# Kernel tuning notes

Hardware: AMD Instinct MI355X
Metric: run time of the kernel (lower is better)

Reference implementation:

```python
import jax, jax.numpy as jnp
import numpy as np
import math

IN_DIM, OUT_DIM, NUM_BASIS = 256, 128, 6
MAX_IN_SEQ, MAX_OUT_SEQ = 512, 256
REDUCTION = 2
LN_EPS = 1e-5


def setup_inputs() -> dict:
    key = jax.random.key(0)
    ks = jax.random.split(key, 8)
    u = lambda k, shape, a: jax.random.uniform(k, shape, jnp.float32, -a, a)
    x = jax.random.normal(ks[0], (16, MAX_IN_SEQ, IN_DIM), jnp.float32)
    M = u(ks[1], (OUT_DIM, IN_DIM), 0.5)
    P = u(ks[2], (OUT_DIM, OUT_DIM, NUM_BASIS), 0.1)
    Linker = u(ks[3], (MAX_IN_SEQ, MAX_OUT_SEQ), 0.1)
    ln_gamma = jnp.ones((OUT_DIM,), jnp.float32)
    ln_beta = jnp.zeros((OUT_DIM,), jnp.float32)
    res_W = u(ks[4], (OUT_DIM, IN_DIM), 0.1)
    res_linker = u(ks[5], (MAX_IN_SEQ, MAX_OUT_SEQ), 0.1)
    # periods[i,j,g] = i*(out_dim*num_basis) + j*num_basis + g + 2 (non-trainable buffer)
    periods = (jnp.arange(OUT_DIM * OUT_DIM * NUM_BASIS, dtype=jnp.float32)
               .reshape(OUT_DIM, OUT_DIM, NUM_BASIS) + 2.0)
    return {"x": x, "M": M, "P": P, "Linker": Linker, "ln_gamma": ln_gamma,
            "ln_beta": ln_beta, "res_W": res_W, "res_linker": res_linker,
            "periods": periods, "actual_seq_len": 512}


def _layer_norm(z, gamma, beta):
    mu = jnp.mean(z, axis=-1, keepdims=True)
    var = jnp.var(z, axis=-1, keepdims=True)
    return (z - mu) * jax.lax.rsqrt(var + LN_EPS) * gamma + beta


def reference(x, M, P, Linker, ln_gamma, ln_beta, res_W, res_linker, periods, actual_seq_len):
    b, seq_len, _ = x.shape
    # Z = LN(x @ M^T)
    Z = _layer_norm(jnp.matmul(x, M.T), ln_gamma, ln_beta)  # (b, s, out)
    # position-dependent trig basis: phi[s,i,j,g] = cos(2*pi*s / periods[i,j,g])
    k = jnp.arange(seq_len, dtype=jnp.float32)[:, None, None, None]
    phi = jnp.cos(2.0 * math.pi * k / periods[None])          # (s, out, out, nb)
    # fold basis into per-position mixing matrix, then contract (matches sum over dims 3,4)
    W = jnp.einsum('ijg,sijg->sij', P, phi)                   # (s, out, out)
    T = jnp.einsum('bsj,sij->bsi', Z, W)                      # (b, s, out)
    # adaptive linker: reduce sequence length
    L = actual_seq_len
    Lo = max(1, L // REDUCTION)
    U = jnp.einsum('bsi,so->boi', T[:, :L], Linker[:L, :Lo])  # (b, out_seq, out)
    # 'separate' residual
    rfeat = jnp.matmul(x[:, :L], res_W.T)                     # (b, s, out)
    residual = jnp.einsum('bsi,so->boi', rfeat, res_linker[:L, :Lo])
    return U + residual
```

## Files before the change

### kernel.cpp

```cpp
#include <hip/hip_runtime.h>
#include <hip/hip_bf16.h>

#define LN_EPS 1e-5f

typedef __attribute__((ext_vector_type(8))) short short8;
typedef __attribute__((ext_vector_type(4))) float floatx4;

__device__ __forceinline__ float bf2f(unsigned int u16) {
    union { unsigned int i; float f; } v; v.i = (u16 & 0xffffu) << 16; return v.f;
}
__device__ __forceinline__ unsigned short f2bf(float f) {
    __hip_bfloat16 h = __float2bfloat16(f);
    union { __hip_bfloat16 h; unsigned short u; } v; v.h = h; return v.u;
}
__device__ __forceinline__ unsigned int pack2(float a, float b) {
    return (unsigned int)f2bf(a) | ((unsigned int)f2bf(b) << 16);
}
__device__ __forceinline__ short8 pack8(float4 a, float4 b) {
    union { short8 s; uint4 u; } v;
    v.u.x = pack2(a.x, a.y); v.u.y = pack2(a.z, a.w);
    v.u.z = pack2(b.x, b.y); v.u.w = pack2(b.z, b.w);
    return v.s;
}

__global__ __launch_bounds__(256) void kB_w_lcat(const float* __restrict__ P,
                                                 const float* __restrict__ periods,
                                                 const float* __restrict__ Linker,
                                                 const float* __restrict__ resL,
                                                 unsigned short* __restrict__ W,
                                                 unsigned short* __restrict__ LcatT) {
    __shared__ unsigned short lds[32 * 260];
    int blk = blockIdx.x, t = threadIdx.x;
    if (blk < 512) {
        int et = blk & 31, sc = blk >> 5;
        int e0 = et * 512 + t * 2;
        const float* pp = P + (size_t)e0 * 6;
        float4 pa = *(const float4*)(pp);
        float4 pb = *(const float4*)(pp + 4);
        float4 pc = *(const float4*)(pp + 8);
        float pf[12] = { pa.x, pa.y, pa.z, pa.w, pb.x, pb.y, pb.z, pb.w, pc.x, pc.y, pc.z, pc.w };
        const float* qp = periods + (size_t)e0 * 6;
        float4 qa = *(const float4*)(qp);
        float4 qb = *(const float4*)(qp + 4);
        float4 qc = *(const float4*)(qp + 8);
        float iv[12] = { __builtin_amdgcn_rcpf(qa.x), __builtin_amdgcn_rcpf(qa.y),
                         __builtin_amdgcn_rcpf(qa.z), __builtin_amdgcn_rcpf(qa.w),
                         __builtin_amdgcn_rcpf(qb.x), __builtin_amdgcn_rcpf(qb.y),
                         __builtin_amdgcn_rcpf(qb.z), __builtin_amdgcn_rcpf(qb.w),
                         __builtin_amdgcn_rcpf(qc.x), __builtin_amdgcn_rcpf(qc.y),
                         __builtin_amdgcn_rcpf(qc.z), __builtin_amdgcn_rcpf(qc.w) };
        float s0 = (float)(sc * 32);
        float tc[12], cm1[12], cc[12];
        #pragma unroll
        for (int g = 0; g < 12; ++g) {
            tc[g]  = 2.0f * __builtin_amdgcn_cosf(iv[g]);
            cm1[g] = __builtin_amdgcn_cosf(__builtin_amdgcn_fractf(s0 * iv[g]));
            cc[g]  = __builtin_amdgcn_cosf(__builtin_amdgcn_fractf((s0 + 1.0f) * iv[g]));
        }
        #pragma unroll 4
        for (int ss = 0; ss < 32; ++ss) {
            float a0 = 0.f, a1 = 0.f;
            #pragma unroll
            for (int g = 0; g < 6; ++g)  a0 += pf[g] * cm1[g];
            #pragma unroll
            for (int g = 6; g < 12; ++g) a1 += pf[g] * cm1[g];
            int s = sc * 32 + ss;
            *(unsigned int*)(W + (size_t)s * 16384 + e0) = pack2(a0, a1);
            #pragma unroll
            for (int g = 0; g < 12; ++g) {
                float cn = fmaf(tc[g], cc[g], -cm1[g]);
                cm1[g] = cc[g]; cc[g] = cn;
            }
        }
    } else {
        int kb = blk - 512;
        int k0 = kb * 32;
        const float* src = (kb < 16) ? (Linker + (size_t)k0 * 256)
                                     : (resL + (size_t)(k0 - 512) * 256);
        #pragma unroll
        for (int q = 0; q < 8; ++q) {
            int lin = t + 256 * q;
            int row = lin >> 6, col4 = (lin & 63) * 4;
            float4 v = *(const float4*)(src + row * 256 + col4);
            *(unsigned int*)(lds + row * 260 + col4)     = pack2(v.x, v.y);
            *(unsigned int*)(lds + row * 260 + col4 + 2) = pack2(v.z, v.w);
        }
        __syncthreads();
        int o = t;
        unsigned int outw[16];
        #pragma unroll
        for (int kp = 0; kp < 16; ++kp) {
            unsigned int lo = lds[(2 * kp) * 260 + o];
            unsigned int hi = lds[(2 * kp + 1) * 260 + o];
            outw[kp] = lo | (hi << 16);
        }
        unsigned short* dst = LcatT + (size_t)o * 1024 + k0;
        #pragma unroll
        for (int qq = 0; qq < 4; ++qq) {
            uint4 u; u.x = outw[qq*4]; u.y = outw[qq*4+1]; u.z = outw[qq*4+2]; u.w = outw[qq*4+3];
            *(uint4*)(dst + qq * 8) = u;
        }
    }
}

__global__ __launch_bounds__(256) void k1_zr(const float* __restrict__ x,
                                             const float* __restrict__ M,
                                             const float* __restrict__ resW,
                                             const float* __restrict__ gamma,
                                             const float* __restrict__ beta,
                                             unsigned short* __restrict__ Z,
                                             unsigned short* __restrict__ TR) {
    __shared__ float buf[32 * 258];
    __shared__ float red1[32 * 8], red2[32 * 8];
    __shared__ float mus[32], rsg[32];
    int t = threadIdx.x, w = t >> 6, l = t & 63;
    int lane15 = l & 15, quad = l >> 4;
    int r0 = blockIdx.x * 32;
    const float* wbase = (w < 2) ? M : resW;
    int wco = (w < 2) ? (w * 64) : (w * 64 - 128);
    floatx4 acc[2][4] = {};
    for (int kk = 0; kk < 256; kk += 32) {
        int k0 = kk + quad * 8;
        const float* xr0 = x + (size_t)(r0 + lane15) * 256 + k0;
        const float* xr1 = x + (size_t)(r0 + 16 + lane15) * 256 + k0;
        short8 a0 = pack8(*(const float4*)xr0, *(const float4*)(xr0 + 4));
        short8 a1 = pack8(*(const float4*)xr1, *(const float4*)(xr1 + 4));
        #pragma unroll
        for (int nt = 0; nt < 4; ++nt) {
            const float* br = wbase + (size_t)(wco + nt * 16 + lane15) * 256 + k0;
            short8 b = pack8(*(const float4*)br, *(const float4*)(br + 4));
            acc[0][nt] = __builtin_amdgcn_mfma_f32_16x16x32_bf16(a0, b, acc[0][nt], 0, 0, 0);
            acc[1][nt] = __builtin_amdgcn_mfma_f32_16x16x32_bf16(a1, b, acc[1][nt], 0, 0, 0);
        }
    }
    #pragma unroll
    for (int mt = 0; mt < 2; ++mt)
        #pragma unroll
        for (int nt = 0; nt < 4; ++nt)
            #pragma unroll
            for (int r = 0; r < 4; ++r) {
                int ro = mt * 16 + quad * 4 + r;
                int co = w * 64 + nt * 16 + lane15;
                buf[ro * 258 + co] = acc[mt][nt][r];
            }
    __syncthreads();
    {
        int r = t >> 3, seg = t & 7;
        float s1 = 0.f, s2 = 0.f;
        #pragma unroll
        for (int e = 0; e < 16; ++e) { float v = buf[r * 258 + seg * 16 + e]; s1 += v; s2 += v * v; }
        red1[r * 8 + seg] = s1; red2[r * 8 + seg] = s2;
    }
    __syncthreads();
    if (t < 32) {
        float s1 = 0.f, s2 = 0.f;
        #pragma unroll
        for (int e = 0; e < 8; ++e) { s1 += red1[t * 8 + e]; s2 += red2[t * 8 + e]; }
        float mu = s1 * (1.0f / 128.0f);
        float var = s2 * (1.0f / 128.0f) - mu * mu;
        mus[t] = mu; rsg[t] = rsqrtf(var + LN_EPS);
    }
    __syncthreads();
    {
        int r = t >> 3, c0 = (t & 7) * 16;
        int grow = r0 + r;
        float mu = mus[r], rs = rsg[r];
        float zv[16], rv[16];
        #pragma unroll
        for (int e = 0; e < 16; ++e) {
            int j = c0 + e;
            zv[e] = (buf[r * 258 + j] - mu) * rs * gamma[j] + beta[j];
            rv[e] = buf[r * 258 + 128 + j];
        }
        uint4 oz0, oz1, or0, or1;
        oz0.x = pack2(zv[0], zv[1]);  oz0.y = pack2(zv[2], zv[3]);
        oz0.z = pack2(zv[4], zv[5]);  oz0.w = pack2(zv[6], zv[7]);
        oz1.x = pack2(zv[8], zv[9]);  oz1.y = pack2(zv[10], zv[11]);
        oz1.z = pack2(zv[12], zv[13]); oz1.w = pack2(zv[14], zv[15]);
        or0.x = pack2(rv[0], rv[1]);  or0.y = pack2(rv[2], rv[3]);
        or0.z = pack2(rv[4], rv[5]);  or0.w = pack2(rv[6], rv[7]);
        or1.x = pack2(rv[8], rv[9]);  or1.y = pack2(rv[10], rv[11]);
        or1.z = pack2(rv[12], rv[13]); or1.w = pack2(rv[14], rv[15]);
        *(uint4*)(Z + (size_t)grow * 128 + c0) = oz0;
        *(uint4*)(Z + (size_t)grow * 128 + c0 + 8) = oz1;
        int b = grow >> 9, s = grow & 511;
        size_t rbase = ((size_t)b * 1024 + 512 + s) * 128 + c0;
        *(uint4*)(TR + rbase) = or0;
        *(uint4*)(TR + rbase + 8) = or1;
    }
}

__global__ __launch_bounds__(64) void k2b_t(const unsigned short* __restrict__ W,
                                            const unsigned short* __restrict__ Z,
                                            unsigned short* __restrict__ TR) {
    int l = threadIdx.x, lane15 = l & 15, quad = l >> 4;
    int s = blockIdx.x;
    floatx4 acc[8] = {};
    #pragma unroll
    for (int kk = 0; kk < 4; ++kk) {
        int k0 = kk * 32 + quad * 8;
        short8 a = *(const short8*)(Z + ((size_t)lane15 * 512 + s) * 128 + k0);
        #pragma unroll
        for (int nt = 0; nt < 8; ++nt) {
            short8 b = *(const short8*)(W + (size_t)s * 16384 + (nt * 16 + lane15) * 128 + k0);
            acc[nt] = __builtin_amdgcn_mfma_f32_16x16x32_bf16(a, b, acc[nt], 0, 0, 0);
        }
    }
    #pragma unroll
    for (int nt = 0; nt < 8; ++nt)
        #pragma unroll
        for (int r = 0; r < 4; ++r) {
            int brow = quad * 4 + r;
            int i = nt * 16 + lane15;
            TR[((size_t)brow * 1024 + s) * 128 + i] = f2bf(acc[nt][r]);
        }
}

__global__ __launch_bounds__(256) void k3_out(const unsigned short* __restrict__ LcatT,
                                              const unsigned short* __restrict__ TR,
                                              float* __restrict__ out) {
    __shared__ unsigned short bt[4][64 * 40];
    __shared__ float red[4 * 32 * 64];
    int t = threadIdx.x, w = t >> 6, l = t & 63;
    int lane15 = l & 15, quad = l >> 4;
    int b = blockIdx.x, o0 = blockIdx.y * 32, i0 = blockIdx.z * 64;
    const unsigned short* trb = TR + (size_t)b * 1024 * 128;
    unsigned short* myBt = bt[w];
    floatx4 acc[2][4] = {};
    for (int kk = 0; kk < 8; ++kk) {
        int k0 = w * 256 + kk * 32;
        __syncthreads();
        {
            int kr = l & 31, ih = (l >> 5) * 8;
            #pragma unroll
            for (int q = 0; q < 4; ++q) {
                int ic = ih + q * 16;
                uint4 u = *(const uint4*)(trb + (size_t)(k0 + kr) * 128 + i0 + ic);
                const unsigned short* up = (const unsigned short*)&u;
                #pragma unroll
                for (int e = 0; e < 8; ++e) myBt[(ic + e) * 40 + kr] = up[e];
            }
        }
        __syncthreads();
        short8 afr0 = *(const short8*)(LcatT + (size_t)(o0 + lane15) * 1024 + k0 + quad * 8);
        short8 afr1 = *(const short8*)(LcatT + (size_t)(o0 + 16 + lane15) * 1024 + k0 + quad * 8);
        #pragma unroll
        for (int nt = 0; nt < 4; ++nt) {
            short8 bfr = *(const short8*)(myBt + (nt * 16 + lane15) * 40 + quad * 8);
            acc[0][nt] = __builtin_amdgcn_mfma_f32_16x16x32_bf16(afr0, bfr, acc[0][nt], 0, 0, 0);
            acc[1][nt] = __builtin_amdgcn_mfma_f32_16x16x32_bf16(afr1, bfr, acc[1][nt], 0, 0, 0);
        }
    }
    #pragma unroll
    for (int mt = 0; mt < 2; ++mt)
        #pragma unroll
        for (int nt = 0; nt < 4; ++nt)
            #pragma unroll
            for (int r = 0; r < 4; ++r) {
                int ro = mt * 16 + quad * 4 + r;
                int co = nt * 16 + lane15;
                red[(w * 32 + ro) * 64 + co] = acc[mt][nt][r];
            }
    __syncthreads();
    {
        int ro = t >> 3, c0 = (t & 7) * 8;
        float vs[8];
        #pragma unroll
        for (int e = 0; e < 8; ++e) {
            float sum = 0.f;
            #pragma unroll
            for (int ww = 0; ww < 4; ++ww) sum += red[(ww * 32 + ro) * 64 + c0 + e];
            vs[e] = sum;
        }
        float4 o1 = { vs[0], vs[1], vs[2], vs[3] };
        float4 o2 = { vs[4], vs[5], vs[6], vs[7] };
        size_t ob = ((size_t)b * 256 + o0 + ro) * 128 + i0 + c0;
        *(float4*)(out + ob) = o1;
        *(float4*)(out + ob + 4) = o2;
    }
}

extern "C" void kernel_launch(void* const* d_in, const int* in_sizes, int n_in,
                              void* d_out, int out_size, void* d_ws, size_t ws_size,
                              hipStream_t stream) {
    const float* x      = (const float*)d_in[0];
    const float* M      = (const float*)d_in[1];
    const float* P      = (const float*)d_in[2];
    const float* Linker = (const float*)d_in[3];
    const float* gamma  = (const float*)d_in[4];
    const float* beta   = (const float*)d_in[5];
    const float* resW   = (const float*)d_in[6];
    const float* resL   = (const float*)d_in[7];
    const float* periods= (const float*)d_in[8];
    (void)in_sizes; (void)n_in; (void)out_size; (void)ws_size;

    float* ws = (float*)d_ws;
    unsigned short* LcatT = (unsigned short*)(ws);
    unsigned short* Z     = (unsigned short*)(ws + 131072);
    unsigned short* TR    = (unsigned short*)(ws + 655360);
    unsigned short* W     = (unsigned short*)(ws + 1703936);

    kB_w_lcat<<<544, 256, 0, stream>>>(P, periods, Linker, resL, W, LcatT);
    k1_zr<<<256, 256, 0, stream>>>(x, M, resW, gamma, beta, Z, TR);
    k2b_t<<<512, 64, 0, stream>>>(W, Z, TR);
    k3_out<<<dim3(16, 8, 2), 256, 0, stream>>>(LcatT, TR, (float*)d_out);
}
```

Baseline: 121.7 us.

## Store intermediate TR transposed so the final GEMM reads B fragments directly

The intermediate T/residual buffer is now written in a [b][i][s] transposed layout by both the Z/residual kernel and the per-position mixing kernel. This lets the final linker GEMM load MFMA B fragments straight from global memory, removing the LDS transpose staging and its two barriers per k-step. The mixing kernel also goes from one wave per position to four waves, each handling 32 output columns, for more parallelism. The catch is that k2b_t now writes scattered 2-byte stores with a 1024-element stride, which makes those writes poorly coalesced.

```diff
diff --git a/kernel.cpp b/kernel.cpp
--- a/kernel.cpp
+++ b/kernel.cpp
@@ -23,7 +23,7 @@
     return v.s;
 }
 
-__global__ __launch_bounds__(256) void kB_w_lcat(const float* __restrict__ P,
+__global__ __launch_bounds__(256) void kA_w_lcat(const float* __restrict__ P,
                                                  const float* __restrict__ periods,
                                                  const float* __restrict__ Linker,
                                                  const float* __restrict__ resL,
@@ -109,7 +109,7 @@
                                              const float* __restrict__ gamma,
                                              const float* __restrict__ beta,
                                              unsigned short* __restrict__ Z,
-                                             unsigned short* __restrict__ TR) {
+                                             unsigned short* __restrict__ TRt) {
     __shared__ float buf[32 * 258];
     __shared__ float red1[32 * 8], red2[32 * 8];
     __shared__ float mus[32], rsg[32];
@@ -161,92 +161,88 @@
         mus[t] = mu; rsg[t] = rsqrtf(var + LN_EPS);
     }
     __syncthreads();
+    int b = r0 >> 9, s0 = r0 & 511;
     {
         int r = t >> 3, c0 = (t & 7) * 16;
         int grow = r0 + r;
         float mu = mus[r], rs = rsg[r];
-        float zv[16], rv[16];
+        float zv[16];
         #pragma unroll
         for (int e = 0; e < 16; ++e) {
             int j = c0 + e;
             zv[e] = (buf[r * 258 + j] - mu) * rs * gamma[j] + beta[j];
-            rv[e] = buf[r * 258 + 128 + j];
-        }
-        uint4 oz0, oz1, or0, or1;
+        }
+        uint4 oz0, oz1;
         oz0.x = pack2(zv[0], zv[1]);  oz0.y = pack2(zv[2], zv[3]);
         oz0.z = pack2(zv[4], zv[5]);  oz0.w = pack2(zv[6], zv[7]);
         oz1.x = pack2(zv[8], zv[9]);  oz1.y = pack2(zv[10], zv[11]);
         oz1.z = pack2(zv[12], zv[13]); oz1.w = pack2(zv[14], zv[15]);
-        or0.x = pack2(rv[0], rv[1]);  or0.y = pack2(rv[2], rv[3]);
-        or0.z = pack2(rv[4], rv[5]);  or0.w = pack2(rv[6], rv[7]);
-        or1.x = pack2(rv[8], rv[9]);  or1.y = pack2(rv[10], rv[11]);
-        or1.z = pack2(rv[12], rv[13]); or1.w = pack2(rv[14], rv[15]);
         *(uint4*)(Z + (size_t)grow * 128 + c0) = oz0;
         *(uint4*)(Z + (size_t)grow * 128 + c0 + 8) = oz1;
-        int b = grow >> 9, s = grow & 511;
-        size_t rbase = ((size_t)b * 1024 + 512 + s) * 128 + c0;
-        *(uint4*)(TR + rbase) = or0;
-        *(uint4*)(TR + rbase + 8) = or1;
-    }
-}
-
-__global__ __launch_bounds__(64) void k2b_t(const unsigned short* __restrict__ W,
-                                            const unsigned short* __restrict__ Z,
-                                            unsigned short* __restrict__ TR) {
-    int l = threadIdx.x, lane15 = l & 15, quad = l >> 4;
+    }
+    {
+        int j = t >> 1, sh = (t & 1) * 16;
+        unsigned int ow[8];
+        #pragma unroll
+        for (int p = 0; p < 8; ++p) {
+            float v0 = buf[(sh + 2 * p) * 258 + 128 + j];
+            float v1 = buf[(sh + 2 * p + 1) * 258 + 128 + j];
+            ow[p] = pack2(v0, v1);
+        }
+        unsigned short* dst = TRt + ((size_t)b * 128 + j) * 1024 + 512 + s0 + sh;
+        uint4 u0; u0.x = ow[0]; u0.y = ow[1]; u0.z = ow[2]; u0.w = ow[3];
+        uint4 u1; u1.x = ow[4]; u1.y = ow[5]; u1.z = ow[6]; u1.w = ow[7];
+        *(uint4*)(dst) = u0;
+        *(uint4*)(dst + 8) = u1;
+    }
+}
+
+__global__ __launch_bounds__(256) void k2b_t(const unsigned short* __restrict__ W,
+                                             const unsigned short* __restrict__ Z,
+                                             unsigned short* __restrict__ TRt) {
+    int t = threadIdx.x, w = t >> 6, l = t & 63;
+    int lane15 = l & 15, quad = l >> 4;
     int s = blockIdx.x;
-    floatx4 acc[8] = {};
+    int i0w = w * 32;
+    floatx4 acc[2] = {};
     #pragma unroll
     for (int kk = 0; kk < 4; ++kk) {
         int k0 = kk * 32 + quad * 8;
         short8 a = *(const short8*)(Z + ((size_t)lane15 * 512 + s) * 128 + k0);
         #pragma unroll
-        for (int nt = 0; nt < 8; ++nt) {
-            short8 b = *(const short8*)(W + (size_t)s * 16384 + (nt * 16 + lane15) * 128 + k0);
-            acc[nt] = __builtin_amdgcn_mfma_f32_16x16x32_bf16(a, b, acc[nt], 0, 0, 0);
+        for (int nt = 0; nt < 2; ++nt) {
+            short8 bf = *(const short8*)(W + (size_t)s * 16384 + (i0w + nt * 16 + lane15) * 128 + k0);
+            acc[nt] = __builtin_amdgcn_mfma_f32_16x16x32_bf16(a, bf, acc[nt], 0, 0, 0);
         }
     }
     #pragma unroll
-    for (int nt = 0; nt < 8; ++nt)
+    for (int nt = 0; nt < 2; ++nt) {
+        int i = i0w + nt * 16 + lane15;
         #pragma unroll
         for (int r = 0; r < 4; ++r) {
             int brow = quad * 4 + r;
-            int i = nt * 16 + lane15;
-            TR[((size_t)brow * 1024 + s) * 128 + i] = f2bf(acc[nt][r]);
-        }
+            TRt[((size_t)brow * 128 + i) * 1024 + s] = f2bf(acc[nt][r]);
+        }
+    }
 }
 
 __global__ __launch_bounds__(256) void k3_out(const unsigned short* __restrict__ LcatT,
-                                              const unsigned short* __restrict__ TR,
+                                              const unsigned short* __restrict__ TRt,
                                               float* __restrict__ out) {
-    __shared__ unsigned short bt[4][64 * 40];
     __shared__ float red[4 * 32 * 64];
     int t = threadIdx.x, w = t >> 6, l = t & 63;
     int lane15 = l & 15, quad = l >> 4;
     int b = blockIdx.x, o0 = blockIdx.y * 32, i0 = blockIdx.z * 64;
-    const unsigned short* trb = TR + (size_t)b * 1024 * 128;
-    unsigned short* myBt = bt[w];
+    const unsigned short* trb = TRt + (size_t)b * 128 * 1024;
     floatx4 acc[2][4] = {};
+    #pragma unroll 2
     for (int kk = 0; kk < 8; ++kk) {
-        int k0 = w * 256 + kk * 32;
-        __syncthreads();
-        {
-            int kr = l & 31, ih = (l >> 5) * 8;
-            #pragma unroll
-            for (int q = 0; q < 4; ++q) {
-                int ic = ih + q * 16;
-                uint4 u = *(const uint4*)(trb + (size_t)(k0 + kr) * 128 + i0 + ic);
-                const unsigned short* up = (const unsigned short*)&u;
-                #pragma unroll
-                for (int e = 0; e < 8; ++e) myBt[(ic + e) * 40 + kr] = up[e];
-            }
-        }
-        __syncthreads();
-        short8 afr0 = *(const short8*)(LcatT + (size_t)(o0 + lane15) * 1024 + k0 + quad * 8);
-        short8 afr1 = *(const short8*)(LcatT + (size_t)(o0 + 16 + lane15) * 1024 + k0 + quad * 8);
+        int k0 = w * 256 + kk * 32 + quad * 8;
+        short8 afr0 = *(const short8*)(LcatT + (size_t)(o0 + lane15) * 1024 + k0);
+        short8 afr1 = *(const short8*)(LcatT + (size_t)(o0 + 16 + lane15) * 1024 + k0);
         #pragma unroll
         for (int nt = 0; nt < 4; ++nt) {
-            short8 bfr = *(const short8*)(myBt + (nt * 16 + lane15) * 40 + quad * 8);
+            short8 bfr = *(const short8*)(trb + (size_t)(i0 + nt * 16 + lane15) * 1024 + k0);
             acc[0][nt] = __builtin_amdgcn_mfma_f32_16x16x32_bf16(afr0, bfr, acc[0][nt], 0, 0, 0);
             acc[1][nt] = __builtin_amdgcn_mfma_f32_16x16x32_bf16(afr1, bfr, acc[1][nt], 0, 0, 0);
         }
@@ -297,11 +293,11 @@
     float* ws = (float*)d_ws;
     unsigned short* LcatT = (unsigned short*)(ws);
     unsigned short* Z     = (unsigned short*)(ws + 131072);
-    unsigned short* TR    = (unsigned short*)(ws + 655360);
+    unsigned short* TRt   = (unsigned short*)(ws + 655360);
     unsigned short* W     = (unsigned short*)(ws + 1703936);
 
-    kB_w_lcat<<<544, 256, 0, stream>>>(P, periods, Linker, resL, W, LcatT);
-    k1_zr<<<256, 256, 0, stream>>>(x, M, resW, gamma, beta, Z, TR);
-    k2b_t<<<512, 64, 0, stream>>>(W, Z, TR);
-    k3_out<<<dim3(16, 8, 2), 256, 0, stream>>>(LcatT, TR, (float*)d_out);
-}
+    kA_w_lcat<<<544, 256, 0, stream>>>(P, periods, Linker, resL, W, LcatT);
+    k1_zr<<<256, 256, 0, stream>>>(x, M, resW, gamma, beta, Z, TRt);
+    k2b_t<<<512, 256, 0, stream>>>(W, Z, TRt);
+    k3_out<<<dim3(16, 8, 2), 256, 0, stream>>>(LcatT, TRt, (float*)d_out);
+}
```

Result: no change. 121.7 us (-0.1%).
